# Kernel tuning notes

Measured on AMD Instinct MI355X. Metric: run time of the kernel, lower is better.

The kernel has to match this reference:

```python
import jax, jax.numpy as jnp
import numpy as np

L, B, S, H = 4, 2, 2048, 1024
NH, HD, FFN = 16, 64, 4096
EPS = 1e-5


def setup_inputs() -> dict:
    key = jax.random.key(0)
    ks = jax.random.split(key, 6)
    std = 0.02
    return {
        "hidden_states": jax.random.normal(ks[0], (B, S, H), jnp.float32),
        "ln1_g": jnp.ones((L, H), jnp.float32),
        "ln1_b": jnp.zeros((L, H), jnp.float32),
        "Wqkv": jax.random.normal(ks[1], (L, H, 3 * H), jnp.float32) * std,
        "Wproj": jax.random.normal(ks[2], (L, H, H), jnp.float32) * std,
        "ln2_g": jnp.ones((L, H), jnp.float32),
        "ln2_b": jnp.zeros((L, H), jnp.float32),
        "Wfc1": jax.random.normal(ks[3], (L, H, FFN), jnp.float32) * std,
        "Wfc2": jax.random.normal(ks[4], (L, FFN, H), jnp.float32) * std,
        "lnf_g": jnp.ones((H,), jnp.float32),
        "lnf_b": jnp.zeros((H,), jnp.float32),
    }


def _layernorm(x, g, b):
    mu = jnp.mean(x, axis=-1, keepdims=True)
    var = jnp.mean(jnp.square(x - mu), axis=-1, keepdims=True)
    return (x - mu) * jax.lax.rsqrt(var + EPS) * g + b


def _block_forward(x, ln1_g, ln1_b, Wqkv, Wproj, ln2_g, ln2_b, Wfc1, Wfc2, lnf_g, lnf_b):
    scale = HD ** -0.5
    causal = jnp.tril(jnp.ones((S, S), bool))  # [S, S]

    def layer(x, p):
        g1, b1, wqkv, wproj, g2, b2, wfc1, wfc2 = p
        # Attention sub-block (pre-norm)
        h = _layernorm(x, g1, b1)
        qkv = (h @ wqkv).reshape(B, S, 3, NH, HD)
        q, k, v = qkv[:, :, 0], qkv[:, :, 1], qkv[:, :, 2]  # [B,S,NH,HD]
        scores = jnp.einsum("bqhd,bkhd->bhqk", q, k) * scale
        scores = jnp.where(causal, scores, -jnp.inf)
        probs = jax.nn.softmax(scores, axis=-1)
        attn = jnp.einsum("bhqk,bkhd->bqhd", probs, v).reshape(B, S, H)
        x = x + attn @ wproj
        # FFN sub-block (pre-norm)
        h = _layernorm(x, g2, b2)
        h = jax.nn.gelu(h @ wfc1, approximate=False) @ wfc2
        return x + h, None

    x, _ = jax.lax.scan(layer, x, (ln1_g, ln1_b, Wqkv, Wproj, ln2_g, ln2_b, Wfc1, Wfc2))
    return _layernorm(x, lnf_g, lnf_b)


def reference(hidden_states, ln1_g, ln1_b, Wqkv, Wproj, ln2_g, ln2_b, Wfc1, Wfc2, lnf_g, lnf_b):
    return _block_forward(hidden_states, ln1_g, ln1_b, Wqkv, Wproj, ln2_g, ln2_b, Wfc1, Wfc2, lnf_g, lnf_b)
```

## Files before the change

### kernel.cpp

```cpp
#include <hip/hip_runtime.h>
#include <hip/hip_bf16.h>
#include <math.h>

#define LYRS 4
#define BB   2
#define SS   2048
#define HH   1024
#define NHD  16
#define HDD  64
#define FFN_ 4096
#define BS   (BB*SS)
#define EPS_ 1e-5f

typedef __attribute__((ext_vector_type(8))) __bf16 bf16x8;
typedef __attribute__((ext_vector_type(4))) __bf16 bf16x4;
typedef __attribute__((ext_vector_type(4))) float f32x4;
typedef __attribute__((address_space(1))) void* gas_t;
typedef __attribute__((address_space(3))) void* las_t;

__device__ inline void async16(void* lds, const void* g) {
    __builtin_amdgcn_global_load_lds((gas_t)g, (las_t)lds, 16, 0, 0);
}

__device__ inline void storev(float* p, float v) { *p = v; }
__device__ inline void storev(__hip_bfloat16* p, float v) { *p = __float2bfloat16(v); }

template <typename OutT>
__global__ void ln_k(const float* __restrict__ x, const float* __restrict__ g,
                     const float* __restrict__ b, OutT* __restrict__ y) {
    const int row = blockIdx.x;
    const int tid = threadIdx.x;
    const float* xr = x + (size_t)row * HH;

    float v[4];
    float s = 0.f, s2 = 0.f;
#pragma unroll
    for (int i = 0; i < 4; ++i) {
        v[i] = xr[tid + i * 256];
        s  += v[i];
        s2 += v[i] * v[i];
    }
#pragma unroll
    for (int o = 1; o < 64; o <<= 1) {
        s  += __shfl_xor(s,  o);
        s2 += __shfl_xor(s2, o);
    }
    __shared__ float sh[8];
    const int wave = tid >> 6, lane = tid & 63;
    if (lane == 0) { sh[wave] = s; sh[4 + wave] = s2; }
    __syncthreads();
    if (tid == 0) {
        float ts  = sh[0] + sh[1] + sh[2] + sh[3];
        float ts2 = sh[4] + sh[5] + sh[6] + sh[7];
        float mu  = ts * (1.f / HH);
        sh[0] = mu;
        sh[1] = ts2 * (1.f / HH) - mu * mu;
    }
    __syncthreads();
    const float mu   = sh[0];
    const float rstd = rsqrtf(sh[1] + EPS_);
#pragma unroll
    for (int i = 0; i < 4; ++i) {
        int c = tid + i * 256;
        storev(&y[(size_t)row * HH + c], (v[i] - mu) * rstd * g[c] + b[c]);
    }
}

__global__ __launch_bounds__(256) void transpose_cast(const float* __restrict__ W,
                                                      __hip_bfloat16* __restrict__ WT,
                                                      int K, int N) {
    __shared__ float t[32][33];
    const int n0 = blockIdx.x * 32, k0 = blockIdx.y * 32;
    const int tx = threadIdx.x & 31, ty8 = threadIdx.x >> 5;
#pragma unroll
    for (int i = 0; i < 4; ++i) {
        int k = ty8 + i * 8;
        t[k][tx] = W[(size_t)(k0 + k) * N + n0 + tx];
    }
    __syncthreads();
#pragma unroll
    for (int i = 0; i < 4; ++i) {
        int n = ty8 + i * 8;
        WT[(size_t)(n0 + n) * K + k0 + tx] = __float2bfloat16(t[tx][n]);
    }
}

template <bool GELU, bool RES, typename OutT>
__global__ __launch_bounds__(256) void gemm_bf16(
    const __hip_bfloat16* __restrict__ A,
    const __hip_bfloat16* __restrict__ BT,
    const float* __restrict__ R,
    OutT* __restrict__ C,
    int M, int N, int K)
{
    __shared__ unsigned short As[128 * 32];
    __shared__ unsigned short Bs[128 * 32];

    const int tid  = threadIdx.x;
    const int lane = tid & 63;
    const int wv   = tid >> 6;
    const int wy   = wv >> 1, wx = wv & 1;
    const int row0 = blockIdx.y * 128;
    const int col0 = blockIdx.x * 128;
    const int lm   = lane & 15;
    const int kq   = lane >> 4;

    const unsigned short* Ag = (const unsigned short*)A;
    const unsigned short* Bg = (const unsigned short*)BT;

    f32x4 acc[4][4] = {};

    for (int k0 = 0; k0 < K; k0 += 32) {
        __syncthreads();
#pragma unroll
        for (int it = 0; it < 2; ++it) {
            int li = it * 256 + tid;
            int r = li >> 2, c = (li & 3) << 3;
            async16(&As[li * 8], &Ag[(size_t)(row0 + r) * K + k0 + c]);
            async16(&Bs[li * 8], &Bg[(size_t)(col0 + r) * K + k0 + c]);
        }
        __syncthreads();

        bf16x8 af[4], bfr[4];
#pragma unroll
        for (int i = 0; i < 4; ++i)
            af[i] = *(const bf16x8*)&As[(wy * 64 + i * 16 + lm) * 32 + kq * 8];
#pragma unroll
        for (int j = 0; j < 4; ++j)
            bfr[j] = *(const bf16x8*)&Bs[(wx * 64 + j * 16 + lm) * 32 + kq * 8];
#pragma unroll
        for (int i = 0; i < 4; ++i)
#pragma unroll
            for (int j = 0; j < 4; ++j)
                acc[i][j] = __builtin_amdgcn_mfma_f32_16x16x32_bf16(
                    af[i], bfr[j], acc[i][j], 0, 0, 0);
    }

#pragma unroll
    for (int i = 0; i < 4; ++i) {
#pragma unroll
        for (int j = 0; j < 4; ++j) {
            int gc = col0 + wx * 64 + j * 16 + lm;
#pragma unroll
            for (int r = 0; r < 4; ++r) {
                int gr = row0 + wy * 64 + i * 16 + kq * 4 + r;
                float v = acc[i][j][r];
                if (RES)  v += R[(size_t)gr * N + gc];
                if (GELU) v = 0.5f * v * (1.0f + erff(v * 0.70710678118654752f));
                storev(&C[(size_t)gr * N + gc], v);
            }
        }
    }
}

__global__ __launch_bounds__(256) void attn_fa3(const __bf16* __restrict__ qkv,
                                                __bf16* __restrict__ out) {
    __shared__ __bf16 Ks[64 * 72];
    __shared__ __bf16 Vt[64 * 72];
    __shared__ __bf16 Ps[4][2][16 * 72];

    const int tid  = threadIdx.x;
    const int lane = tid & 63;
    const int w    = tid >> 6;
    const int lm   = lane & 15;
    const int kq   = lane >> 4;

    const int x  = blockIdx.x;
    const int bh = x & 31;
    const int h  = bh & 15;
    const int b  = bh >> 4;
    const int a  = (x >> 5) & 7;
    const int qt = (x & 256) ? (15 - a) : a;
    const int q0 = qt * 128;

    const size_t rs   = 3 * HH;
    const size_t base = (size_t)b * SS * rs + (size_t)h * HDD;

    bf16x8 qf[2][2];
#pragma unroll
    for (int s = 0; s < 2; ++s)
#pragma unroll
        for (int kh = 0; kh < 2; ++kh) {
            bf16x8 t = *(const bf16x8*)&qkv[base +
                (size_t)(q0 + w * 32 + s * 16 + lm) * rs + kh * 32 + kq * 8];
#pragma unroll
            for (int j = 0; j < 8; ++j) t[j] = (__bf16)((float)t[j] * 0.125f);
            qf[s][kh] = t;
        }

    f32x4 ot[2][4] = {};
    float m_i[2] = {-INFINITY, -INFINITY};
    float l_i[2] = {0.f, 0.f};

    const int qmax_w = q0 + w * 32 + 31;
    const int ktmax  = (q0 + 127) >> 6;

    for (int kt = 0; kt <= ktmax; ++kt) {
        const int k0 = kt << 6;
        __syncthreads();
#pragma unroll
        for (int it = 0; it < 2; ++it) {
            int li  = it * 256 + tid;
            int row = li >> 3, c = (li & 7) << 3;
            *(bf16x8*)&Ks[row * 72 + c] =
                *(const bf16x8*)&qkv[base + (size_t)(k0 + row) * rs + HH + c];
        }
#pragma unroll
        for (int it = 0; it < 2; ++it) {
            int li  = it * 256 + tid;
            int key = li & 63, cb = (li >> 6) << 3;
            bf16x8 v = *(const bf16x8*)&qkv[base + (size_t)(k0 + key) * rs + 2 * HH + cb];
#pragma unroll
            for (int j = 0; j < 8; ++j) Vt[(cb + j) * 72 + key] = v[j];
        }
        __syncthreads();

        if (k0 > qmax_w) continue;

#pragma unroll
        for (int s = 0; s < 2; ++s) {
            f32x4 st[4] = {};
#pragma unroll
            for (int kh = 0; kh < 2; ++kh)
#pragma unroll
                for (int m = 0; m < 4; ++m) {
                    bf16x8 kf = *(const bf16x8*)&Ks[(m * 16 + lm) * 72 + kh * 32 + kq * 8];
                    st[m] = __builtin_amdgcn_mfma_f32_16x16x32_bf16(
                        kf, qf[s][kh], st[m], 0, 0, 0);
                }

            const int qg = q0 + w * 32 + s * 16 + lm;
            if (k0 + 63 > q0 + w * 32 + s * 16) {
#pragma unroll
                for (int m = 0; m < 4; ++m) {
                    int keyb = k0 + m * 16 + kq * 4;
#pragma unroll
                    for (int r = 0; r < 4; ++r)
                        if (keyb + r > qg) st[m][r] = -INFINITY;
                }
            }

            float mloc = -INFINITY;
#pragma unroll
            for (int m = 0; m < 4; ++m)
#pragma unroll
                for (int r = 0; r < 4; ++r) mloc = fmaxf(mloc, st[m][r]);
            mloc = fmaxf(mloc, __shfl_xor(mloc, 16));
            mloc = fmaxf(mloc, __shfl_xor(mloc, 32));
            float mn    = fmaxf(m_i[s], mloc);
            float alpha = __expf(m_i[s] - mn);
            m_i[s] = mn;

            float sum = 0.f;
#pragma unroll
            for (int m = 0; m < 4; ++m) {
                bf16x4 pb;
#pragma unroll
                for (int r = 0; r < 4; ++r) {
                    float p = __expf(st[m][r] - mn);
                    sum += p;
                    pb[r] = (__bf16)p;
                }
                *(bf16x4*)&Ps[w][s][lm * 72 + m * 16 + kq * 4] = pb;
            }
            sum += __shfl_xor(sum, 16);
            sum += __shfl_xor(sum, 32);
            l_i[s] = l_i[s] * alpha + sum;

#pragma unroll
            for (int dt = 0; dt < 4; ++dt) ot[s][dt] *= alpha;

#pragma unroll
            for (int kh = 0; kh < 2; ++kh) {
                bf16x8 pf = *(const bf16x8*)&Ps[w][s][lm * 72 + kh * 32 + kq * 8];
#pragma unroll
                for (int dt = 0; dt < 4; ++dt) {
                    bf16x8 vf = *(const bf16x8*)&Vt[(dt * 16 + lm) * 72 + kh * 32 + kq * 8];
                    ot[s][dt] = __builtin_amdgcn_mfma_f32_16x16x32_bf16(
                        vf, pf, ot[s][dt], 0, 0, 0);
                }
            }
        }
    }

#pragma unroll
    for (int s = 0; s < 2; ++s) {
        float inv = 1.f / l_i[s];
        int qg = q0 + w * 32 + s * 16 + lm;
#pragma unroll
        for (int dt = 0; dt < 4; ++dt) {
            bf16x4 ob;
#pragma unroll
            for (int r = 0; r < 4; ++r) ob[r] = (__bf16)(ot[s][dt][r] * inv);
            *(bf16x4*)&out[(size_t)(b * SS + qg) * HH + h * HDD + dt * 16 + kq * 4] = ob;
        }
    }
}

extern "C" void kernel_launch(void* const* d_in, const int* in_sizes, int n_in,
                              void* d_out, int out_size, void* d_ws, size_t ws_size,
                              hipStream_t stream) {
    const float* hidden = (const float*)d_in[0];
    const float* ln1_g  = (const float*)d_in[1];
    const float* ln1_b  = (const float*)d_in[2];
    const float* Wqkv   = (const float*)d_in[3];
    const float* Wproj  = (const float*)d_in[4];
    const float* ln2_g  = (const float*)d_in[5];
    const float* ln2_b  = (const float*)d_in[6];
    const float* Wfc1   = (const float*)d_in[7];
    const float* Wfc2   = (const float*)d_in[8];
    const float* lnf_g  = (const float*)d_in[9];
    const float* lnf_b  = (const float*)d_in[10];

    float* x = (float*)d_out;

    char* p = (char*)d_ws;
    __hip_bfloat16* hbuf  = (__hip_bfloat16*)p; p += (size_t)BS * HH * 2;
    __hip_bfloat16* qkvb  = (__hip_bfloat16*)p; p += (size_t)BS * 3 * HH * 2;
    __hip_bfloat16* attnb = (__hip_bfloat16*)p; p += (size_t)BS * HH * 2;
    __hip_bfloat16* ffnb  = (__hip_bfloat16*)p; p += (size_t)BS * FFN_ * 2;
    __hip_bfloat16* wqkvT = (__hip_bfloat16*)p; p += (size_t)3 * HH * HH * 2;
    __hip_bfloat16* wprojT= (__hip_bfloat16*)p; p += (size_t)HH * HH * 2;
    __hip_bfloat16* wfc1T = (__hip_bfloat16*)p; p += (size_t)FFN_ * HH * 2;
    __hip_bfloat16* wfc2T = (__hip_bfloat16*)p; p += (size_t)HH * FFN_ * 2;

    hipMemcpyAsync(x, hidden, (size_t)BS * HH * sizeof(float),
                   hipMemcpyDeviceToDevice, stream);

    for (int lyr = 0; lyr < LYRS; ++lyr) {
        transpose_cast<<<dim3(3 * HH / 32, HH / 32), 256, 0, stream>>>(
            Wqkv + (size_t)lyr * HH * 3 * HH, wqkvT, HH, 3 * HH);
        transpose_cast<<<dim3(HH / 32, HH / 32), 256, 0, stream>>>(
            Wproj + (size_t)lyr * HH * HH, wprojT, HH, HH);
        transpose_cast<<<dim3(FFN_ / 32, HH / 32), 256, 0, stream>>>(
            Wfc1 + (size_t)lyr * HH * FFN_, wfc1T, HH, FFN_);
        transpose_cast<<<dim3(HH / 32, FFN_ / 32), 256, 0, stream>>>(
            Wfc2 + (size_t)lyr * FFN_ * HH, wfc2T, FFN_, HH);

        ln_k<__hip_bfloat16><<<BS, 256, 0, stream>>>(
            x, ln1_g + lyr * HH, ln1_b + lyr * HH, hbuf);
        gemm_bf16<false, false, __hip_bfloat16>
            <<<dim3(3 * HH / 128, BS / 128), 256, 0, stream>>>(
            hbuf, wqkvT, nullptr, qkvb, BS, 3 * HH, HH);
        attn_fa3<<<512, 256, 0, stream>>>((const __bf16*)qkvb, (__bf16*)attnb);
        gemm_bf16<false, true, float>
            <<<dim3(HH / 128, BS / 128), 256, 0, stream>>>(
            attnb, wprojT, x, x, BS, HH, HH);
        ln_k<__hip_bfloat16><<<BS, 256, 0, stream>>>(
            x, ln2_g + lyr * HH, ln2_b + lyr * HH, hbuf);
        gemm_bf16<true, false, __hip_bfloat16>
            <<<dim3(FFN_ / 128, BS / 128), 256, 0, stream>>>(
            hbuf, wfc1T, nullptr, ffnb, BS, FFN_, HH);
        gemm_bf16<false, true, float>
            <<<dim3(HH / 128, BS / 128), 256, 0, stream>>>(
            ffnb, wfc2T, x, x, BS, HH, FFN_);
    }
    ln_k<float><<<BS, 256, 0, stream>>>(x, lnf_g, lnf_b, x);
}
```

Before: 1.551 ms.

## Double-buffer K/V tiles in attention and remap GEMM block order column-major

The attention kernel now keeps two LDS buffers for K and V. It prefetches the next tile's K/V into registers while computing on the current tile, then writes them to the other buffer, which removes one barrier per iteration and hides global load latency. The GEMM launches become 1D grids whose block index walks down rows first inside each column tile, so concurrently running blocks share the same weight columns and get better L2 reuse. In exchange, attention uses more LDS and registers, which may lower occupancy.

```diff
diff --git a/kernel.cpp b/kernel.cpp
--- a/kernel.cpp
+++ b/kernel.cpp
@@ -100,8 +100,11 @@
     const int lane = tid & 63;
     const int wv   = tid >> 6;
     const int wy   = wv >> 1, wx = wv & 1;
-    const int row0 = blockIdx.y * 128;
-    const int col0 = blockIdx.x * 128;
+    const int nby  = M >> 7;
+    const int by   = blockIdx.x % nby;
+    const int bx   = blockIdx.x / nby;
+    const int row0 = by * 128;
+    const int col0 = bx * 128;
     const int lm   = lane & 15;
     const int kq   = lane >> 4;
 
@@ -155,8 +158,8 @@
 
 __global__ __launch_bounds__(256) void attn_fa3(const __bf16* __restrict__ qkv,
                                                 __bf16* __restrict__ out) {
-    __shared__ __bf16 Ks[64 * 72];
-    __shared__ __bf16 Vt[64 * 72];
+    __shared__ __bf16 Ks[2][64 * 72];
+    __shared__ __bf16 Vt[2][64 * 72];
     __shared__ __bf16 Ps[4][2][16 * 72];
 
     const int tid  = threadIdx.x;
@@ -176,6 +179,11 @@
     const size_t rs   = 3 * HH;
     const size_t base = (size_t)b * SS * rs + (size_t)h * HDD;
 
+    const int krow0 = tid >> 3,        kc0 = (tid & 7) << 3;
+    const int krow1 = (256 + tid) >> 3, kc1 = ((256 + tid) & 7) << 3;
+    const int vkey  = tid & 63;
+    const int vcb0  = (tid >> 6) << 3, vcb1 = ((256 + tid) >> 6) << 3;
+
     bf16x8 qf[2][2];
 #pragma unroll
     for (int s = 0; s < 2; ++s)
@@ -195,91 +203,110 @@
     const int qmax_w = q0 + w * 32 + 31;
     const int ktmax  = (q0 + 127) >> 6;
 
+    bf16x8 kr0, kr1, vr0, vr1;
+    {
+        const int k0 = 0;
+        kr0 = *(const bf16x8*)&qkv[base + (size_t)(k0 + krow0) * rs + HH + kc0];
+        kr1 = *(const bf16x8*)&qkv[base + (size_t)(k0 + krow1) * rs + HH + kc1];
+        vr0 = *(const bf16x8*)&qkv[base + (size_t)(k0 + vkey) * rs + 2 * HH + vcb0];
+        vr1 = *(const bf16x8*)&qkv[base + (size_t)(k0 + vkey) * rs + 2 * HH + vcb1];
+        *(bf16x8*)&Ks[0][krow0 * 72 + kc0] = kr0;
+        *(bf16x8*)&Ks[0][krow1 * 72 + kc1] = kr1;
+#pragma unroll
+        for (int j = 0; j < 8; ++j) Vt[0][(vcb0 + j) * 72 + vkey] = vr0[j];
+#pragma unroll
+        for (int j = 0; j < 8; ++j) Vt[0][(vcb1 + j) * 72 + vkey] = vr1[j];
+    }
+    __syncthreads();
+
     for (int kt = 0; kt <= ktmax; ++kt) {
-        const int k0 = kt << 6;
-        __syncthreads();
-#pragma unroll
-        for (int it = 0; it < 2; ++it) {
-            int li  = it * 256 + tid;
-            int row = li >> 3, c = (li & 7) << 3;
-            *(bf16x8*)&Ks[row * 72 + c] =
-                *(const bf16x8*)&qkv[base + (size_t)(k0 + row) * rs + HH + c];
-        }
-#pragma unroll
-        for (int it = 0; it < 2; ++it) {
-            int li  = it * 256 + tid;
-            int key = li & 63, cb = (li >> 6) << 3;
-            bf16x8 v = *(const bf16x8*)&qkv[base + (size_t)(k0 + key) * rs + 2 * HH + cb];
-#pragma unroll
-            for (int j = 0; j < 8; ++j) Vt[(cb + j) * 72 + key] = v[j];
-        }
-        __syncthreads();
-
-        if (k0 > qmax_w) continue;
-
-#pragma unroll
-        for (int s = 0; s < 2; ++s) {
-            f32x4 st[4] = {};
-#pragma unroll
-            for (int kh = 0; kh < 2; ++kh)
+        const int k0  = kt << 6;
+        const int buf = kt & 1;
+
+        if (kt < ktmax) {
+            const int kn = k0 + 64;
+            kr0 = *(const bf16x8*)&qkv[base + (size_t)(kn + krow0) * rs + HH + kc0];
+            kr1 = *(const bf16x8*)&qkv[base + (size_t)(kn + krow1) * rs + HH + kc1];
+            vr0 = *(const bf16x8*)&qkv[base + (size_t)(kn + vkey) * rs + 2 * HH + vcb0];
+            vr1 = *(const bf16x8*)&qkv[base + (size_t)(kn + vkey) * rs + 2 * HH + vcb1];
+        }
+
+        if (k0 <= qmax_w) {
+#pragma unroll
+            for (int s = 0; s < 2; ++s) {
+                f32x4 st[4] = {};
+#pragma unroll
+                for (int kh = 0; kh < 2; ++kh)
+#pragma unroll
+                    for (int m = 0; m < 4; ++m) {
+                        bf16x8 kf = *(const bf16x8*)&Ks[buf][(m * 16 + lm) * 72 + kh * 32 + kq * 8];
+                        st[m] = __builtin_amdgcn_mfma_f32_16x16x32_bf16(
+                            kf, qf[s][kh], st[m], 0, 0, 0);
+                    }
+
+                const int qg = q0 + w * 32 + s * 16 + lm;
+                if (k0 + 63 > q0 + w * 32 + s * 16) {
+#pragma unroll
+                    for (int m = 0; m < 4; ++m) {
+                        int keyb = k0 + m * 16 + kq * 4;
+#pragma unroll
+                        for (int r = 0; r < 4; ++r)
+                            if (keyb + r > qg) st[m][r] = -INFINITY;
+                    }
+                }
+
+                float mloc = -INFINITY;
+#pragma unroll
+                for (int m = 0; m < 4; ++m)
+#pragma unroll
+                    for (int r = 0; r < 4; ++r) mloc = fmaxf(mloc, st[m][r]);
+                mloc = fmaxf(mloc, __shfl_xor(mloc, 16));
+                mloc = fmaxf(mloc, __shfl_xor(mloc, 32));
+                float mn    = fmaxf(m_i[s], mloc);
+                float alpha = __expf(m_i[s] - mn);
+                m_i[s] = mn;
+
+                float sum = 0.f;
 #pragma unroll
                 for (int m = 0; m < 4; ++m) {
-                    bf16x8 kf = *(const bf16x8*)&Ks[(m * 16 + lm) * 72 + kh * 32 + kq * 8];
-                    st[m] = __builtin_amdgcn_mfma_f32_16x16x32_bf16(
-                        kf, qf[s][kh], st[m], 0, 0, 0);
+                    bf16x4 pb;
+#pragma unroll
+                    for (int r = 0; r < 4; ++r) {
+                        float p = __expf(st[m][r] - mn);
+                        sum += p;
+                        pb[r] = (__bf16)p;
+                    }
+                    *(bf16x4*)&Ps[w][s][lm * 72 + m * 16 + kq * 4] = pb;
                 }
-
-            const int qg = q0 + w * 32 + s * 16 + lm;
-            if (k0 + 63 > q0 + w * 32 + s * 16) {
-#pragma unroll
-                for (int m = 0; m < 4; ++m) {
-                    int keyb = k0 + m * 16 + kq * 4;
-#pragma unroll
-                    for (int r = 0; r < 4; ++r)
-                        if (keyb + r > qg) st[m][r] = -INFINITY;
+                sum += __shfl_xor(sum, 16);
+                sum += __shfl_xor(sum, 32);
+                l_i[s] = l_i[s] * alpha + sum;
+
+#pragma unroll
+                for (int dt = 0; dt < 4; ++dt) ot[s][dt] *= alpha;
+
+#pragma unroll
+                for (int kh = 0; kh < 2; ++kh) {
+                    bf16x8 pf = *(const bf16x8*)&Ps[w][s][lm * 72 + kh * 32 + kq * 8];
+#pragma unroll
+                    for (int dt = 0; dt < 4; ++dt) {
+                        bf16x8 vf = *(const bf16x8*)&Vt[buf][(dt * 16 + lm) * 72 + kh * 32 + kq * 8];
+                        ot[s][dt] = __builtin_amdgcn_mfma_f32_16x16x32_bf16(
+                            vf, pf, ot[s][dt], 0, 0, 0);
+                    }
                 }
             }
-
-            float mloc = -INFINITY;
-#pragma unroll
-            for (int m = 0; m < 4; ++m)
-#pragma unroll
-                for (int r = 0; r < 4; ++r) mloc = fmaxf(mloc, st[m][r]);
-            mloc = fmaxf(mloc, __shfl_xor(mloc, 16));
-            mloc = fmaxf(mloc, __shfl_xor(mloc, 32));
-            float mn    = fmaxf(m_i[s], mloc);
-            float alpha = __expf(m_i[s] - mn);
-            m_i[s] = mn;
-
-            float sum = 0.f;
-#pragma unroll
-            for (int m = 0; m < 4; ++m) {
-                bf16x4 pb;
-#pragma unroll
-                for (int r = 0; r < 4; ++r) {
-                    float p = __expf(st[m][r] - mn);
-                    sum += p;
-                    pb[r] = (__bf16)p;
-                }
-                *(bf16x4*)&Ps[w][s][lm * 72 + m * 16 + kq * 4] = pb;
-            }
-            sum += __shfl_xor(sum, 16);
-            sum += __shfl_xor(sum, 32);
-            l_i[s] = l_i[s] * alpha + sum;
-
-#pragma unroll
-            for (int dt = 0; dt < 4; ++dt) ot[s][dt] *= alpha;
-
-#pragma unroll
-            for (int kh = 0; kh < 2; ++kh) {
-                bf16x8 pf = *(const bf16x8*)&Ps[w][s][lm * 72 + kh * 32 + kq * 8];
-#pragma unroll
-                for (int dt = 0; dt < 4; ++dt) {
-                    bf16x8 vf = *(const bf16x8*)&Vt[(dt * 16 + lm) * 72 + kh * 32 + kq * 8];
-                    ot[s][dt] = __builtin_amdgcn_mfma_f32_16x16x32_bf16(
-                        vf, pf, ot[s][dt], 0, 0, 0);
-                }
-            }
+        }
+
+        if (kt < ktmax) {
+            const int nb = buf ^ 1;
+            *(bf16x8*)&Ks[nb][krow0 * 72 + kc0] = kr0;
+            *(bf16x8*)&Ks[nb][krow1 * 72 + kc1] = kr1;
+#pragma unroll
+            for (int j = 0; j < 8; ++j) Vt[nb][(vcb0 + j) * 72 + vkey] = vr0[j];
+#pragma unroll
+            for (int j = 0; j < 8; ++j) Vt[nb][(vcb1 + j) * 72 + vkey] = vr1[j];
+            __syncthreads();
         }
     }
 
@@ -327,6 +354,8 @@
     hipMemcpyAsync(x, hidden, (size_t)BS * HH * sizeof(float),
                    hipMemcpyDeviceToDevice, stream);
 
+    const int NBY = BS / 128;
+
     for (int lyr = 0; lyr < LYRS; ++lyr) {
         transpose_cast<<<dim3(3 * HH / 32, HH / 32), 256, 0, stream>>>(
             Wqkv + (size_t)lyr * HH * 3 * HH, wqkvT, HH, 3 * HH);
@@ -340,19 +369,19 @@
         ln_k<__hip_bfloat16><<<BS, 256, 0, stream>>>(
             x, ln1_g + lyr * HH, ln1_b + lyr * HH, hbuf);
         gemm_bf16<false, false, __hip_bfloat16>
-            <<<dim3(3 * HH / 128, BS / 128), 256, 0, stream>>>(
+            <<<(3 * HH / 128) * NBY, 256, 0, stream>>>(
             hbuf, wqkvT, nullptr, qkvb, BS, 3 * HH, HH);
         attn_fa3<<<512, 256, 0, stream>>>((const __bf16*)qkvb, (__bf16*)attnb);
         gemm_bf16<false, true, float>
-            <<<dim3(HH / 128, BS / 128), 256, 0, stream>>>(
+            <<<(HH / 128) * NBY, 256, 0, stream>>>(
             attnb, wprojT, x, x, BS, HH, HH);
         ln_k<__hip_bfloat16><<<BS, 256, 0, stream>>>(
             x, ln2_g + lyr * HH, ln2_b + lyr * HH, hbuf);
         gemm_bf16<true, false, __hip_bfloat16>
-            <<<dim3(FFN_ / 128, BS / 128), 256, 0, stream>>>(
+            <<<(FFN_ / 128) * NBY, 256, 0, stream>>>(
             hbuf, wfc1T, nullptr, ffnb, BS, FFN_, HH);
         gemm_bf16<false, true, float>
-            <<<dim3(HH / 128, BS / 128), 256, 0, stream>>>(
+            <<<(HH / 128) * NBY, 256, 0, stream>>>(
             ffnb, wfc2T, x, x, BS, HH, FFN_);
     }
     ln_k<float><<<BS, 256, 0, stream>>>(x, lnf_g, lnf_b, x);
```

After: 1.406 ms. -9.3%, faster.
